# Optimization experiments

Hardware: AMD Instinct MI355X
Metric: run time of the kernel (lower is better)

Reference implementation:

```python
import jax, jax.numpy as jnp
import numpy as np

EPS = 1e-5
INV_TEMP = 100.0  # sim / 0.01


def _center_norm(x):
    # x: [B, C, S]; per-segment channel mean-centering + L2 norm over channels
    xm = x - jnp.mean(x, axis=1, keepdims=True)
    return xm / (jnp.linalg.norm(xm, axis=1, keepdims=True) + EPS)


def setup_inputs() -> dict:
    key = jax.random.key(0)
    ks = jax.random.split(key, 12)
    B, C, S = 16, 128, 2048  # S = max_segments + 1
    H = W = 64
    wscale = 1.0 / np.sqrt(C)
    return {
        "cat_encoded_target": jax.random.normal(ks[0], (B, C, S), jnp.float32),
        "cat_encoded_ref": jax.random.normal(ks[1], (B, C, S), jnp.float32),
        "label_mask_target": jax.random.randint(ks[2], (B, 1, H, W), 0, 2047, jnp.int32),
        "label_mask_ref": jax.random.randint(ks[3], (B, 1, H, W), 0, 2047, jnp.int32),
        "input_features_in": jax.random.normal(ks[4], (B, C, 8, 8), jnp.float32),
        "max_segments": 2047,
        "cat_encoded_rgb_ref": jax.random.normal(ks[5], (B, C, S), jnp.float32),
        "max_segments_ref": 2047,
        "device": 0,
        "Wq": jax.random.normal(ks[6], (C, C), jnp.float32) * wscale,
        "bq": jax.random.normal(ks[7], (C,), jnp.float32) * 0.01,
        "Wk": jax.random.normal(ks[8], (C, C), jnp.float32) * wscale,
        "bk": jax.random.normal(ks[9], (C,), jnp.float32) * 0.01,
        "Wv": jax.random.normal(ks[10], (C, C), jnp.float32) * wscale,
        "bv": jax.random.normal(ks[11], (C,), jnp.float32) * 0.01,
    }


def reference(cat_encoded_target, cat_encoded_ref, label_mask_target,
              label_mask_ref, input_features_in, max_segments,
              cat_encoded_rgb_ref, max_segments_ref, device,
              Wq, bq, Wk, bk, Wv, bv):
    B = cat_encoded_target.shape[0]
    Np1 = max_segments + 1
    Mp1 = max_segments_ref + 1

    # per-sample ragged lengths from label maps (vectorized instead of host sync)
    label_t = jnp.max(label_mask_target.reshape(B, -1), axis=1) + 1  # [B]
    label_r = jnp.max(label_mask_ref.reshape(B, -1), axis=1) + 1     # [B]
    row_mask = jnp.arange(Np1)[None, :] < label_t[:, None]           # [B, Np1]
    col_mask = jnp.arange(Mp1)[None, :] < label_r[:, None]           # [B, Mp1]

    # 1x1 convs == per-segment channel matmul + bias
    q = jnp.einsum('oc,bcn->bon', Wq, _center_norm(cat_encoded_target)) + bq[None, :, None]
    k = jnp.einsum('oc,bcm->bom', Wk, _center_norm(cat_encoded_ref)) + bk[None, :, None]
    v = jnp.einsum('oc,bcm->bom', Wv, cat_encoded_rgb_ref) + bv[None, :, None]

    sim = jnp.einsum('bcn,bcm->bnm', q, k) * INV_TEMP  # [B, Np1, Mp1]
    # mask invalid ref columns to -inf (exactly 0 after softmax, matching zero-padding),
    # zero invalid target rows (they were never written in the original)
    att = jax.nn.softmax(jnp.where(col_mask[:, None, :], sim, -jnp.inf), axis=2)
    att = att * row_mask[:, :, None].astype(att.dtype)

    wg_ref = jnp.einsum('bnm,bcm->bnc', att, v)  # [B, Np1, C]; invalid rows -> 0
    return jnp.transpose(wg_ref, (0, 2, 1)), att
```

## Files before the change

### kernel.cpp

```cpp
#include <hip/hip_runtime.h>
#include <math.h>

constexpr int NB = 16;
constexpr int NC = 128;
constexpr int NS = 2048;
constexpr float F_INV_TEMP = 100.0f;
constexpr float F_EPS = 1e-5f;
constexpr float NEGBIG = -1e30f;

typedef __attribute__((ext_vector_type(8))) _Float16 f16x8;
typedef __attribute__((ext_vector_type(4))) _Float16 f16x4;
typedef __attribute__((ext_vector_type(4))) float f32x4;

#define MFMA16(a, b, c) __builtin_amdgcn_mfma_f32_16x16x32_f16((a), (b), (c), 0, 0, 0)

constexpr size_t F16_OFF = 64;
constexpr size_t QT_H   = 0;
constexpr size_t KT_H   = QT_H + (size_t)NB * NS * NC;
constexpr size_t VT_H   = KT_H + (size_t)NB * NS * NC;
constexpr size_t W16_H  = VT_H + (size_t)NB * NS * NC;

__global__ void k_lens(const int* __restrict__ lm_t, const int* __restrict__ lm_r,
                       int* __restrict__ lens) {
    int b = blockIdx.x & 15;
    const int* src = (blockIdx.x < 16) ? lm_t : lm_r;
    src += b * 4096;
    int m = 0;
    for (int i = threadIdx.x; i < 4096; i += 256) m = max(m, src[i]);
    for (int off = 32; off; off >>= 1) m = max(m, __shfl_down(m, off, 64));
    __shared__ int red[4];
    if ((threadIdx.x & 63) == 0) red[threadIdx.x >> 6] = m;
    __syncthreads();
    if (threadIdx.x == 0) {
        m = max(max(red[0], red[1]), max(red[2], red[3]));
        lens[blockIdx.x] = m + 1;
    }
}

__global__ void k_prep(const float* __restrict__ Wq, const float* __restrict__ Wk,
                       const float* __restrict__ Wv, _Float16* __restrict__ W16) {
    int i = blockIdx.x * 256 + threadIdx.x;
    W16[i]               = (_Float16)Wq[i];
    W16[i + NC * NC]     = (_Float16)Wk[i];
    W16[i + 2 * NC * NC] = (_Float16)Wv[i];
}

template <bool NORM, int MODE>
__global__ __launch_bounds__(256) void k_qkv(const float* __restrict__ x,
                                             const _Float16* __restrict__ W16,
                                             const float* __restrict__ bias,
                                             _Float16* __restrict__ out,
                                             _Float16* __restrict__ vout) {
    __shared__ __align__(16) char smem[48 * 1024];
    float*    xs = (float*)smem;
    _Float16* xn = (_Float16*)(smem + 32 * 1024);
    _Float16 (*Vt)[72] = (_Float16 (*)[72])smem;
    __shared__ float ps[4][64], pq[4][64], cmean[64], cscale[64];

    const int b  = blockIdx.y;
    const int s0 = blockIdx.x * 64;
    const float* xb = x + (size_t)b * NC * NS + s0;

    for (int idx = threadIdx.x; idx < NC * 16; idx += 256) {
        int c = idx >> 4, j = (idx & 15) << 2;
        *(float4*)&xs[c * 64 + j] = *(const float4*)&xb[(size_t)c * NS + j];
    }
    __syncthreads();

    if (NORM) {
        int j = threadIdx.x & 63, p = threadIdx.x >> 6;
        float sum = 0.f, ssq = 0.f;
#pragma unroll
        for (int cc = 0; cc < 32; ++cc) {
            float v = xs[(p * 32 + cc) * 64 + j];
            sum += v; ssq += v * v;
        }
        ps[p][j] = sum; pq[p][j] = ssq;
        __syncthreads();
        if (threadIdx.x < 64) {
            float sm = ps[0][j] + ps[1][j] + ps[2][j] + ps[3][j];
            float sq = pq[0][j] + pq[1][j] + pq[2][j] + pq[3][j];
            float mean = sm * (1.f / NC);
            float var = sq - (float)NC * mean * mean;
            cmean[j]  = mean;
            cscale[j] = 1.f / (sqrtf(fmaxf(var, 0.f)) + F_EPS);
        }
        __syncthreads();
    }

    {
        const int lane = threadIdx.x & 63;
        const int w4   = threadIdx.x >> 6;
        const float mn = NORM ? cmean[lane] : 0.f;
        const float sc = NORM ? cscale[lane] : 1.f;
#pragma unroll
        for (int q = 0; q < 4; ++q) {
            f16x8 v8;
#pragma unroll
            for (int i = 0; i < 8; ++i)
                v8[i] = (_Float16)((xs[(w4 * 32 + q * 8 + i) * 64 + lane] - mn) * sc);
            *(f16x8*)(xn + lane * 128 + (((w4 * 4 + q) ^ (lane & 7)) << 3)) = v8;
        }
    }
    __syncthreads();

    const int w = threadIdx.x >> 6, lane = threadIdx.x & 63;
    const int ln = lane & 15, g = lane >> 4;
    const int sl = w * 16 + ln;

    f16x8 xf[4];
#pragma unroll
    for (int jj = 0; jj < 4; ++jj)
        xf[jj] = *(const f16x8*)(xn + sl * 128 + (((jj * 4 + g) ^ (ln & 7)) << 3));

#pragma unroll
    for (int ot = 0; ot < 8; ++ot) {
        const _Float16* wrow = W16 + (size_t)(ot * 16 + ln) * NC + g * 8;
        f32x4 acc = {0.f, 0.f, 0.f, 0.f};
        acc = MFMA16(*(const f16x8*)(wrow),      xf[0], acc);
        acc = MFMA16(*(const f16x8*)(wrow + 32), xf[1], acc);
        acc = MFMA16(*(const f16x8*)(wrow + 64), xf[2], acc);
        acc = MFMA16(*(const f16x8*)(wrow + 96), xf[3], acc);
        const float4 bv = *(const float4*)&bias[ot * 16 + 4 * g];
        f16x4 res;
        res[0] = (_Float16)(acc[0] + bv.x);
        res[1] = (_Float16)(acc[1] + bv.y);
        res[2] = (_Float16)(acc[2] + bv.z);
        res[3] = (_Float16)(acc[3] + bv.w);
        if (MODE < 2) {
            *(f16x4*)(out + ((size_t)b * NS + s0 + sl) * NC + ot * 16 + 4 * g) = res;
        } else {
#pragma unroll
            for (int r = 0; r < 4; ++r)
                Vt[ot * 16 + 4 * g + r][sl] = res[r];
        }
    }
    if (MODE == 2) {
        __syncthreads();
        int o = threadIdx.x >> 1, sh = threadIdx.x & 1;
        _Float16* vr = vout + ((size_t)b * NC + o) * NS + s0 + sh * 32;
        const _Float16* src = &Vt[o][sh * 32];
#pragma unroll
        for (int i = 0; i < 4; ++i) *(f16x8*)(vr + i * 8) = *(const f16x8*)(src + i * 8);
    }
}

__global__ __launch_bounds__(512, 4) void k_attn(const _Float16* __restrict__ qt,
                                                 const _Float16* __restrict__ kt,
                                                 const _Float16* __restrict__ vt,
                                                 const int* __restrict__ lens,
                                                 float* __restrict__ att,
                                                 float* __restrict__ out0) {
    __shared__ _Float16 Klds[64 * 128];
    __shared__ _Float16 Vlds[128 * 64];
    __shared__ _Float16 Plds[8][16][40];
    const int nt = blockIdx.x, b = blockIdx.y;
    const int tid = threadIdx.x;
    const int w = tid >> 6, lane = tid & 63, ln = lane & 15, g = lane >> 4;
    const int n_base = nt * 128 + w * 16;
    const int lenq = lens[b], lenr = lens[16 + b];
    const int swz = ln & 7;

    const _Float16* qrow = qt + ((size_t)b * NS + n_base + ln) * NC + g * 8;
    f16x8 qf[4];
#pragma unroll
    for (int j = 0; j < 4; ++j) qf[j] = *(const f16x8*)(qrow + 32 * j);

    const _Float16* kb = kt + (size_t)b * NS * NC;
    const _Float16* vb = vt + (size_t)b * NC * NS;

    f16x8 kreg[2], vreg[2];
    auto load_k = [&](int mg0) {
#pragma unroll
        for (int q = 0; q < 2; ++q) {
            int idx = q * 512 + tid;
            kreg[q] = *(const f16x8*)(kb + (size_t)(mg0 + (idx >> 4)) * NC + (idx & 15) * 8);
        }
    };
    auto store_k = [&]() {
#pragma unroll
        for (int q = 0; q < 2; ++q) {
            int idx = q * 512 + tid;
            int r = idx >> 4, s = idx & 15;
            *(f16x8*)(Klds + r * 128 + ((s ^ (r & 7)) << 3)) = kreg[q];
        }
    };
    auto load_v = [&](int mg0) {
#pragma unroll
        for (int q = 0; q < 2; ++q) {
            int idx = q * 512 + tid;
            vreg[q] = *(const f16x8*)(vb + (size_t)(idx >> 3) * NS + mg0 + (idx & 7) * 8);
        }
    };
    auto store_v = [&]() {
#pragma unroll
        for (int q = 0; q < 2; ++q) {
            int idx = q * 512 + tid;
            int rv = idx >> 3, sv = idx & 7;
            *(f16x8*)(Vlds + rv * 64 + ((sv ^ (rv & 7)) << 3)) = vreg[q];
        }
    };

    float mrun = NEGBIG, srun = 0.f;
    const int NT1 = (lenr + 63) >> 6;
    load_k(0);
    for (int it = 0; it < NT1; ++it) {
        const int mg0 = it * 64;
        __syncthreads();
        store_k();
        if (it + 1 < NT1) load_k(mg0 + 64);
        __syncthreads();
#pragma unroll
        for (int half = 0; half < 2; ++half) {
            const int m0 = half * 32;
            f32x4 a0 = {0.f, 0.f, 0.f, 0.f}, a1 = {0.f, 0.f, 0.f, 0.f};
#pragma unroll
            for (int j = 0; j < 4; ++j) {
                f16x8 k0 = *(const f16x8*)(Klds + (m0 + ln) * 128 + ((((j << 2) + g) ^ swz) << 3));
                f16x8 k1 = *(const f16x8*)(Klds + (m0 + 16 + ln) * 128 + ((((j << 2) + g) ^ swz) << 3));
                a0 = MFMA16(k0, qf[j], a0);
                a1 = MFMA16(k1, qf[j], a1);
            }
            float vv[8];
#pragma unroll
            for (int r = 0; r < 4; ++r) {
                int mi = mg0 + m0 + 4 * g + r;
                vv[r]     = (mi      < lenr) ? a0[r] * F_INV_TEMP : NEGBIG;
                vv[4 + r] = (mi + 16 < lenr) ? a1[r] * F_INV_TEMP : NEGBIG;
            }
            float cmax = fmaxf(fmaxf(fmaxf(vv[0], vv[1]), fmaxf(vv[2], vv[3])),
                               fmaxf(fmaxf(vv[4], vv[5]), fmaxf(vv[6], vv[7])));
            float newm = fmaxf(mrun, cmax);
            float ssum = 0.f;
#pragma unroll
            for (int i = 0; i < 8; ++i) ssum += __expf(vv[i] - newm);
            srun = srun * __expf(mrun - newm) + ssum;
            mrun = newm;
        }
    }
#pragma unroll
    for (int off = 16; off <= 32; off <<= 1) {
        float om = __shfl_xor(mrun, off, 64);
        float os = __shfl_xor(srun, off, 64);
        float nm = fmaxf(mrun, om);
        srun = srun * __expf(mrun - nm) + os * __expf(om - nm);
        mrun = nm;
    }
    const float M = mrun;
    const float rinv = ((n_base + ln) < lenq) ? (1.0f / srun) : 0.0f;

    f32x4 opv[8];
#pragma unroll
    for (int ct = 0; ct < 8; ++ct) opv[ct] = f32x4{0.f, 0.f, 0.f, 0.f};

    float* attb = att + ((size_t)b * NS + n_base + ln) * NS;

    constexpr int NT = NS / 64;
    load_k(0); load_v(0);
    for (int it = 0; it < NT; ++it) {
        const int mg0 = it * 64;
        const bool live = (mg0 < lenr);
        __syncthreads();
        if (live) { store_k(); store_v(); }
        if (it + 1 < NT) { load_k(mg0 + 64); load_v(mg0 + 64); }
        __syncthreads();
        if (!live) {
            f32x4 z = {0.f, 0.f, 0.f, 0.f};
#pragma unroll
            for (int h = 0; h < 4; ++h)
                *(f32x4*)(attb + mg0 + h * 16 + 4 * g) = z;
            continue;
        }
#pragma unroll
        for (int half = 0; half < 2; ++half) {
            const int m0 = half * 32;
            f32x4 a0 = {0.f, 0.f, 0.f, 0.f}, a1 = {0.f, 0.f, 0.f, 0.f};
#pragma unroll
            for (int j = 0; j < 4; ++j) {
                f16x8 k0 = *(const f16x8*)(Klds + (m0 + ln) * 128 + ((((j << 2) + g) ^ swz) << 3));
                f16x8 k1 = *(const f16x8*)(Klds + (m0 + 16 + ln) * 128 + ((((j << 2) + g) ^ swz) << 3));
                a0 = MFMA16(k0, qf[j], a0);
                a1 = MFMA16(k1, qf[j], a1);
            }
            f32x4 p0, p1;
#pragma unroll
            for (int r = 0; r < 4; ++r) {
                int mi = mg0 + m0 + 4 * g + r;
                float v0 = (mi      < lenr) ? a0[r] * F_INV_TEMP : NEGBIG;
                float v1 = (mi + 16 < lenr) ? a1[r] * F_INV_TEMP : NEGBIG;
                p0[r] = __expf(v0 - M) * rinv;
                p1[r] = __expf(v1 - M) * rinv;
            }
            *(f32x4*)(attb + mg0 + m0 + 4 * g)      = p0;
            *(f32x4*)(attb + mg0 + m0 + 16 + 4 * g) = p1;

            f16x4 pk0, pk1;
#pragma unroll
            for (int r = 0; r < 4; ++r) {
                pk0[r] = (_Float16)p0[r];
                pk1[r] = (_Float16)p1[r];
            }
            *(f16x4*)&Plds[w][ln][4 * g]      = pk0;
            *(f16x4*)&Plds[w][ln][16 + 4 * g] = pk1;
            f16x8 pf = *(const f16x8*)&Plds[w][ln][g * 8];

#pragma unroll
            for (int ct = 0; ct < 8; ++ct) {
                f16x8 vf = *(const f16x8*)(Vlds + (ct * 16 + ln) * 64 +
                                           (((half * 4 + g) ^ swz) << 3));
                opv[ct] = MFMA16(pf, vf, opv[ct]);
            }
        }
    }

    float* ob = out0 + (size_t)b * NC * NS;
#pragma unroll
    for (int ct = 0; ct < 8; ++ct)
        *(f32x4*)(ob + (size_t)(ct * 16 + ln) * NS + n_base + 4 * g) = opv[ct];
}

extern "C" void kernel_launch(void* const* d_in, const int* in_sizes, int n_in,
                              void* d_out, int out_size, void* d_ws, size_t ws_size,
                              hipStream_t stream) {
    const float* xt   = (const float*)d_in[0];
    const float* xr   = (const float*)d_in[1];
    const int*   lmt  = (const int*)d_in[2];
    const int*   lmr  = (const int*)d_in[3];
    const float* xrgb = (const float*)d_in[6];
    const float* Wq   = (const float*)d_in[9];
    const float* bq   = (const float*)d_in[10];
    const float* Wk   = (const float*)d_in[11];
    const float* bk   = (const float*)d_in[12];
    const float* Wv   = (const float*)d_in[13];
    const float* bv   = (const float*)d_in[14];

    float* out0 = (float*)d_out;
    float* att  = out0 + (size_t)NB * NC * NS;

    float* ws   = (float*)d_ws;
    int*   lens = (int*)d_ws;
    _Float16* h = (_Float16*)(ws + F16_OFF);
    _Float16* qt  = h + QT_H;
    _Float16* kt  = h + KT_H;
    _Float16* vt  = h + VT_H;
    _Float16* W16 = h + W16_H;

    k_lens<<<32, 256, 0, stream>>>(lmt, lmr, lens);
    k_prep<<<NC * NC / 256, 256, 0, stream>>>(Wq, Wk, Wv, W16);

    dim3 gproj(NS / 64, NB);
    k_qkv<true,  0><<<gproj, 256, 0, stream>>>(xt,   W16,               bq, qt, nullptr);
    k_qkv<true,  1><<<gproj, 256, 0, stream>>>(xr,   W16 + NC * NC,     bk, kt, nullptr);
    k_qkv<false, 2><<<gproj, 256, 0, stream>>>(xrgb, W16 + 2 * NC * NC, bv, nullptr, vt);

    dim3 gattn(NS / 128, NB);
    k_attn<<<gattn, 512, 0, stream>>>(qt, kt, vt, lens, att, out0);
}
```

Baseline: 165.4 us.

## Stage attention probabilities in LDS and write coalesced full rows

Attention probabilities are buffered per 256-column group in a shared f16 tile, then written to global memory as contiguous row segments by each wave instead of scattered 16-byte stores. This targets inefficient store coalescing on the large att output. It adds LDS usage, an extra barrier per group, and reduces launch bounds occupancy to 2 blocks; stored att values are now rounded through f16, reducing precision.

```diff
diff --git a/kernel.cpp b/kernel.cpp
--- a/kernel.cpp
+++ b/kernel.cpp
@@ -145,7 +145,8 @@
     }
 }
 
-__global__ __launch_bounds__(512, 4) void k_attn(const _Float16* __restrict__ qt,
+constexpr int ATS = 264;
+__global__ __launch_bounds__(512, 2) void k_attn(const _Float16* __restrict__ qt,
                                                  const _Float16* __restrict__ kt,
                                                  const _Float16* __restrict__ vt,
                                                  const int* __restrict__ lens,
@@ -154,12 +155,14 @@
     __shared__ _Float16 Klds[64 * 128];
     __shared__ _Float16 Vlds[128 * 64];
     __shared__ _Float16 Plds[8][16][40];
+    __shared__ _Float16 AttH[128 * ATS];
     const int nt = blockIdx.x, b = blockIdx.y;
     const int tid = threadIdx.x;
     const int w = tid >> 6, lane = tid & 63, ln = lane & 15, g = lane >> 4;
     const int n_base = nt * 128 + w * 16;
     const int lenq = lens[b], lenr = lens[16 + b];
     const int swz = ln & 7;
+    const int rloc = w * 16 + ln;
 
     const _Float16* qrow = qt + ((size_t)b * NS + n_base + ln) * NC + g * 8;
     f16x8 qf[4];
@@ -253,62 +256,79 @@
 #pragma unroll
     for (int ct = 0; ct < 8; ++ct) opv[ct] = f32x4{0.f, 0.f, 0.f, 0.f};
 
-    float* attb = att + ((size_t)b * NS + n_base + ln) * NS;
-
-    constexpr int NT = NS / 64;
+    const f16x4 z4 = {(_Float16)0.f, (_Float16)0.f, (_Float16)0.f, (_Float16)0.f};
+    float* attrow0 = att + ((size_t)b * NS + nt * 128) * NS;
+
     load_k(0); load_v(0);
-    for (int it = 0; it < NT; ++it) {
-        const int mg0 = it * 64;
-        const bool live = (mg0 < lenr);
-        __syncthreads();
-        if (live) { store_k(); store_v(); }
-        if (it + 1 < NT) { load_k(mg0 + 64); load_v(mg0 + 64); }
-        __syncthreads();
-        if (!live) {
-            f32x4 z = {0.f, 0.f, 0.f, 0.f};
-#pragma unroll
-            for (int h = 0; h < 4; ++h)
-                *(f32x4*)(attb + mg0 + h * 16 + 4 * g) = z;
-            continue;
-        }
-#pragma unroll
-        for (int half = 0; half < 2; ++half) {
-            const int m0 = half * 32;
-            f32x4 a0 = {0.f, 0.f, 0.f, 0.f}, a1 = {0.f, 0.f, 0.f, 0.f};
-#pragma unroll
-            for (int j = 0; j < 4; ++j) {
-                f16x8 k0 = *(const f16x8*)(Klds + (m0 + ln) * 128 + ((((j << 2) + g) ^ swz) << 3));
-                f16x8 k1 = *(const f16x8*)(Klds + (m0 + 16 + ln) * 128 + ((((j << 2) + g) ^ swz) << 3));
-                a0 = MFMA16(k0, qf[j], a0);
-                a1 = MFMA16(k1, qf[j], a1);
-            }
-            f32x4 p0, p1;
-#pragma unroll
-            for (int r = 0; r < 4; ++r) {
-                int mi = mg0 + m0 + 4 * g + r;
-                float v0 = (mi      < lenr) ? a0[r] * F_INV_TEMP : NEGBIG;
-                float v1 = (mi + 16 < lenr) ? a1[r] * F_INV_TEMP : NEGBIG;
-                p0[r] = __expf(v0 - M) * rinv;
-                p1[r] = __expf(v1 - M) * rinv;
-            }
-            *(f32x4*)(attb + mg0 + m0 + 4 * g)      = p0;
-            *(f32x4*)(attb + mg0 + m0 + 16 + 4 * g) = p1;
-
-            f16x4 pk0, pk1;
-#pragma unroll
-            for (int r = 0; r < 4; ++r) {
-                pk0[r] = (_Float16)p0[r];
-                pk1[r] = (_Float16)p1[r];
-            }
-            *(f16x4*)&Plds[w][ln][4 * g]      = pk0;
-            *(f16x4*)&Plds[w][ln][16 + 4 * g] = pk1;
-            f16x8 pf = *(const f16x8*)&Plds[w][ln][g * 8];
-
-#pragma unroll
-            for (int ct = 0; ct < 8; ++ct) {
-                f16x8 vf = *(const f16x8*)(Vlds + (ct * 16 + ln) * 64 +
-                                           (((half * 4 + g) ^ swz) << 3));
-                opv[ct] = MFMA16(pf, vf, opv[ct]);
+    for (int gi = 0; gi < 8; ++gi) {
+#pragma unroll
+        for (int tt = 0; tt < 4; ++tt) {
+            const int it = gi * 4 + tt;
+            const int mg0 = it * 64;
+            const int ttm = tt * 64;
+            const bool live = (mg0 < lenr);
+            __syncthreads();
+            if (live) { store_k(); store_v(); }
+            if (it + 1 < 32) { load_k(mg0 + 64); load_v(mg0 + 64); }
+            __syncthreads();
+            if (!live) {
+#pragma unroll
+                for (int h = 0; h < 4; ++h)
+                    *(f16x4*)&AttH[rloc * ATS + ttm + h * 16 + 4 * g] = z4;
+                continue;
+            }
+#pragma unroll
+            for (int half = 0; half < 2; ++half) {
+                const int m0 = half * 32;
+                f32x4 a0 = {0.f, 0.f, 0.f, 0.f}, a1 = {0.f, 0.f, 0.f, 0.f};
+#pragma unroll
+                for (int j = 0; j < 4; ++j) {
+                    f16x8 k0 = *(const f16x8*)(Klds + (m0 + ln) * 128 + ((((j << 2) + g) ^ swz) << 3));
+                    f16x8 k1 = *(const f16x8*)(Klds + (m0 + 16 + ln) * 128 + ((((j << 2) + g) ^ swz) << 3));
+                    a0 = MFMA16(k0, qf[j], a0);
+                    a1 = MFMA16(k1, qf[j], a1);
+                }
+                f32x4 p0, p1;
+#pragma unroll
+                for (int r = 0; r < 4; ++r) {
+                    int mi = mg0 + m0 + 4 * g + r;
+                    float v0 = (mi      < lenr) ? a0[r] * F_INV_TEMP : NEGBIG;
+                    float v1 = (mi + 16 < lenr) ? a1[r] * F_INV_TEMP : NEGBIG;
+                    p0[r] = __expf(v0 - M) * rinv;
+                    p1[r] = __expf(v1 - M) * rinv;
+                }
+                f16x4 pk0, pk1;
+#pragma unroll
+                for (int r = 0; r < 4; ++r) {
+                    pk0[r] = (_Float16)p0[r];
+                    pk1[r] = (_Float16)p1[r];
+                }
+                *(f16x4*)&AttH[rloc * ATS + ttm + m0 + 4 * g]      = pk0;
+                *(f16x4*)&AttH[rloc * ATS + ttm + m0 + 16 + 4 * g] = pk1;
+                *(f16x4*)&Plds[w][ln][4 * g]      = pk0;
+                *(f16x4*)&Plds[w][ln][16 + 4 * g] = pk1;
+                f16x8 pf = *(const f16x8*)&Plds[w][ln][g * 8];
+
+#pragma unroll
+                for (int ct = 0; ct < 8; ++ct) {
+                    f16x8 vf = *(const f16x8*)(Vlds + (ct * 16 + ln) * 64 +
+                                               (((half * 4 + g) ^ swz) << 3));
+                    opv[ct] = MFMA16(pf, vf, opv[ct]);
+                }
+            }
+        }
+        __syncthreads();
+        {
+            float* fgb = attrow0 + gi * 256;
+            const int c4 = lane * 4;
+#pragma unroll
+            for (int pass = 0; pass < 16; ++pass) {
+                const int rr = w * 16 + pass;
+                f16x4 hv = *(const f16x4*)&AttH[rr * ATS + c4];
+                f32x4 fv;
+                fv[0] = (float)hv[0]; fv[1] = (float)hv[1];
+                fv[2] = (float)hv[2]; fv[3] = (float)hv[3];
+                *(f32x4*)(fgb + (size_t)rr * NS + c4) = fv;
             }
         }
     }
```

After: 177.3 us. 7.2% more time.
